# Optimization experiments

Measured on AMD Instinct MI355X. Metric: run time of the kernel, lower is better.

Reference implementation:

```python
import jax, jax.numpy as jnp
import numpy as np

N_ATOMS = 100_000
N_PAIRS = 3_200_000
N_SPECIES = 8
BOX = 5.0


def _sym(key, lo, hi):
    m = jax.random.uniform(key, (N_SPECIES, N_SPECIES), minval=lo, maxval=hi, dtype=jnp.float32)
    return 0.5 * (m + m.T)  # species matrices must be symmetric


def setup_inputs() -> dict:
    key = jax.random.key(0)
    ks = jax.random.split(key, 7)
    positions = jax.random.uniform(ks[0], (N_ATOMS, 3), dtype=jnp.float32) * BOX
    cell = BOX * jnp.eye(3, dtype=jnp.float32)
    i = jax.random.randint(ks[1], (N_PAIRS,), 0, N_ATOMS)
    off = jax.random.randint(ks[2], (N_PAIRS,), 1, N_ATOMS)  # exclude self-pairs (r=0)
    j = (i + off) % N_ATOMS
    mapping = jnp.stack([i, j]).astype(jnp.int64)
    shifts = jnp.zeros((N_PAIRS, 3), dtype=jnp.float32)
    species = jax.random.randint(ks[3], (N_ATOMS,), 0, N_SPECIES).astype(jnp.int64)
    sigma_matrix = _sym(ks[4], 1.0, 2.0)
    epsilon_matrix = _sym(ks[5], 0.5, 1.5)
    alpha_matrix = _sym(ks[6], 2.0, 3.0)
    return dict(positions=positions, cell=cell, sigma_matrix=sigma_matrix,
                epsilon_matrix=epsilon_matrix, alpha_matrix=alpha_matrix,
                shifts=shifts, mapping=mapping, species=species)


def reference(positions, cell, sigma_matrix, epsilon_matrix, alpha_matrix, shifts, mapping, species):
    n = positions.shape[0]
    i, j = mapping[0], mapping[1]
    # pair displacements with periodic shifts: dr = r_j - r_i + S @ cell
    dr = positions[j] - positions[i] + shifts @ cell              # [P,3]
    r = jnp.sqrt(jnp.sum(dr * dr, axis=-1))                       # [P]
    # species-pair parameter lookup
    si, sj = species[i], species[j]
    sigma = sigma_matrix[si, sj]
    eps = epsilon_matrix[si, sj]
    alpha = alpha_matrix[si, sj]
    # soft-sphere pair energy: eps/alpha * (1 - r/sigma)^alpha for r < sigma, else 0
    mask = r < sigma
    base = jnp.where(mask, 1.0 - r / sigma, 1.0)                  # safe base for pow/grad
    e_pair = jnp.where(mask, (eps / alpha) * base ** alpha, 0.0)
    energy = 0.5 * jnp.sum(e_pair)
    energies = (jax.ops.segment_sum(0.5 * e_pair, i, num_segments=n)
                + jax.ops.segment_sum(0.5 * e_pair, j, num_segments=n))
    # pair force magnitude: -dE/dr = eps/sigma * (1 - r/sigma)^(alpha-1)
    f_pair = jnp.where(mask, (eps / sigma) * base ** (alpha - 1.0), 0.0)
    fvec = (f_pair / r)[:, None] * dr                             # [P,3]
    forces = (jax.ops.segment_sum(fvec, i, num_segments=n)
              - jax.ops.segment_sum(fvec, j, num_segments=n))
    # virial stress
    volume = jnp.abs(jnp.linalg.det(cell))
    stress = -jnp.einsum('pi,pj->ij', dr, fvec) / volume          # [3,3]
    return energy, energies, forces, stress
```

## Files before the change

kernel.cpp:

```cpp
#include <hip/hip_runtime.h>
#include <math.h>

#define NSP 8

typedef float v4f __attribute__((ext_vector_type(4)));

#define FSCALE 1048576.0f
#define FINV   (1.0f/1048576.0f)
#define ESCALE 131072.0f
#define EINV   (1.0f/131072.0f)
#define FBIAS  2.0f

__global__ __launch_bounds__(256) void repack_kernel(
    const float* __restrict__ pos, const int* __restrict__ spec,
    v4f* __restrict__ ps, unsigned long long* __restrict__ accum, int n)
{
    int t = blockIdx.x * blockDim.x + threadIdx.x;
    if (t < n) {
        v4f v;
        v.x = pos[3 * t];
        v.y = pos[3 * t + 1];
        v.z = pos[3 * t + 2];
        v.w = __int_as_float(spec[t]);
        ps[t] = v;
        accum[2 * t]     = 0ULL;
        accum[2 * t + 1] = 0ULL;
    }
}

__global__ __launch_bounds__(256, 8) void pair_kernel(
    const v4f* __restrict__ ps,
    const float* __restrict__ cell,
    const float* __restrict__ sigma_m,
    const float* __restrict__ eps_m,
    const float* __restrict__ alpha_m,
    const float* __restrict__ shifts,
    const int* __restrict__ mapping,
    unsigned long long* __restrict__ accum,
    float* __restrict__ partials,
    int n_atoms, int n_pairs)
{
    __shared__ float s_sigma[64], s_invsig[64], s_alpha[64], s_eoa[64], s_eos[64];
    __shared__ float s_cell[9];
    const int t = threadIdx.x;
    if (t < 64) {
        float sg = sigma_m[t], ep = eps_m[t], al = alpha_m[t];
        s_sigma[t]  = sg;
        s_invsig[t] = 1.0f / sg;
        s_alpha[t]  = al;
        s_eoa[t]    = ep / al;
        s_eos[t]    = ep / sg;
    }
    if (t < 9) s_cell[t] = cell[t];
    __syncthreads();

    const int p = blockIdx.x * 256 + t;

    float le = 0.f;
    float s00 = 0.f, s01 = 0.f, s02 = 0.f, s11 = 0.f, s12 = 0.f, s22 = 0.f;

    if (p < n_pairs) {
        const int i = mapping[p];
        const int j = mapping[p + n_pairs];
        const float shx = shifts[3 * p];
        const float shy = shifts[3 * p + 1];
        const float shz = shifts[3 * p + 2];

        const v4f pi = ps[i];
        const v4f pj = ps[j];

        const float drx = pj.x - pi.x + shx * s_cell[0] + shy * s_cell[3] + shz * s_cell[6];
        const float dry = pj.y - pi.y + shx * s_cell[1] + shy * s_cell[4] + shz * s_cell[7];
        const float drz = pj.z - pi.z + shx * s_cell[2] + shy * s_cell[5] + shz * s_cell[8];
        const float r = sqrtf(drx * drx + dry * dry + drz * drz);

        const int idx = __float_as_int(pi.w) * NSP + __float_as_int(pj.w);
        const float sg = s_sigma[idx];
        if (r < sg) {
            const float base = 1.0f - r * s_invsig[idx];
            const float pb   = __powf(base, s_alpha[idx] - 1.0f);
            const float e    = s_eoa[idx] * pb * base;
            const float f    = s_eos[idx] * pb;
            const float sc   = f / r;
            const float fx = sc * drx, fy = sc * dry, fz = sc * drz;

            le  = e;
            s00 = drx * fx; s01 = drx * fy; s02 = drx * fz;
            s11 = dry * fy; s12 = dry * fz; s22 = drz * fz;

            const float he = 0.5f * e;
            const unsigned long long he_fix = (unsigned long long)__float2uint_rn(he * ESCALE);
            {
                const unsigned long long fxq = (unsigned long long)__float2uint_rn((fx + FBIAS) * FSCALE);
                const unsigned long long fyq = (unsigned long long)__float2uint_rn((fy + FBIAS) * FSCALE);
                const unsigned long long fzq = (unsigned long long)__float2uint_rn((fz + FBIAS) * FSCALE);
                atomicAdd(&accum[2 * i],     (fxq << 32) | fyq);
                atomicAdd(&accum[2 * i + 1], (1ULL << 56) | (he_fix << 32) | fzq);
            }
            {
                const unsigned long long fxq = (unsigned long long)__float2uint_rn((FBIAS - fx) * FSCALE);
                const unsigned long long fyq = (unsigned long long)__float2uint_rn((FBIAS - fy) * FSCALE);
                const unsigned long long fzq = (unsigned long long)__float2uint_rn((FBIAS - fz) * FSCALE);
                atomicAdd(&accum[2 * j],     (fxq << 32) | fyq);
                atomicAdd(&accum[2 * j + 1], (1ULL << 56) | (he_fix << 32) | fzq);
            }
        }
    }

    float vals[7] = {le, s00, s01, s02, s11, s12, s22};
    #pragma unroll
    for (int k = 0; k < 7; ++k) {
        float v = vals[k];
        #pragma unroll
        for (int off = 32; off > 0; off >>= 1)
            v += __shfl_down(v, off, 64);
        vals[k] = v;
    }
    __shared__ float s_red[4][7];
    const int wave = t >> 6, lane = t & 63;
    if (lane == 0) {
        #pragma unroll
        for (int k = 0; k < 7; ++k) s_red[wave][k] = vals[k];
    }
    __syncthreads();
    if (t == 0) {
        #pragma unroll
        for (int k = 0; k < 7; ++k) {
            partials[(size_t)blockIdx.x * 8 + k] =
                s_red[0][k] + s_red[1][k] + s_red[2][k] + s_red[3][k];
        }
        partials[(size_t)blockIdx.x * 8 + 7] = 0.f;
    }
}

__global__ __launch_bounds__(256) void reduce_tail(
    const float* __restrict__ partials, float* __restrict__ tail, int nblocks)
{
    const int t = threadIdx.x;
    float acc[7] = {0.f, 0.f, 0.f, 0.f, 0.f, 0.f, 0.f};
    for (int b = t; b < nblocks; b += 256) {
        #pragma unroll
        for (int k = 0; k < 7; ++k) acc[k] += partials[(size_t)b * 8 + k];
    }
    #pragma unroll
    for (int k = 0; k < 7; ++k) {
        float v = acc[k];
        #pragma unroll
        for (int off = 32; off > 0; off >>= 1)
            v += __shfl_down(v, off, 64);
        acc[k] = v;
    }
    __shared__ float s_red[4][7];
    const int wave = t >> 6, lane = t & 63;
    if (lane == 0) {
        #pragma unroll
        for (int k = 0; k < 7; ++k) s_red[wave][k] = acc[k];
    }
    __syncthreads();
    if (t == 0) {
        #pragma unroll
        for (int k = 0; k < 7; ++k)
            tail[k] = s_red[0][k] + s_red[1][k] + s_red[2][k] + s_red[3][k];
    }
}

__global__ __launch_bounds__(256) void finalize_kernel(
    const unsigned long long* __restrict__ accum, const float* __restrict__ tail,
    const float* __restrict__ cell, float* __restrict__ out, int n_atoms)
{
    const int t = blockIdx.x * blockDim.x + threadIdx.x;
    if (t < n_atoms) {
        const unsigned long long A = accum[2 * t];
        const unsigned long long B = accum[2 * t + 1];
        const float cntb = (float)(unsigned)(B >> 56) * FBIAS;
        const float fx = (float)(unsigned)(A >> 32)          * FINV - cntb;
        const float fy = (float)(unsigned)(A & 0xFFFFFFFFu)  * FINV - cntb;
        const float fz = (float)(unsigned)(B & 0xFFFFFFFFu)  * FINV - cntb;
        const float he = (float)(unsigned)((B >> 32) & 0xFFFFFFu) * EINV;
        out[1 + t] = he;
        float* forces = out + 1 + n_atoms;
        forces[3 * t]     = fx;
        forces[3 * t + 1] = fy;
        forces[3 * t + 2] = fz;
    }
    if (t == 0) {
        out[0] = 0.5f * tail[0];
        const float c0 = cell[0], c1 = cell[1], c2 = cell[2];
        const float c3 = cell[3], c4 = cell[4], c5 = cell[5];
        const float c6 = cell[6], c7 = cell[7], c8 = cell[8];
        const float det = c0 * (c4 * c8 - c5 * c7)
                        - c1 * (c3 * c8 - c5 * c6)
                        + c2 * (c3 * c7 - c4 * c6);
        const float nv = -1.0f / fabsf(det);
        float* st = out + 1 + 4 * n_atoms;
        st[0] = tail[1] * nv;  st[1] = tail[2] * nv;  st[2] = tail[3] * nv;
        st[3] = tail[2] * nv;  st[4] = tail[4] * nv;  st[5] = tail[5] * nv;
        st[6] = tail[3] * nv;  st[7] = tail[5] * nv;  st[8] = tail[6] * nv;
    }
}

__global__ __launch_bounds__(256) void soft_sphere_fallback(
    const float* __restrict__ positions, const float* __restrict__ cell,
    const float* __restrict__ sigma_m, const float* __restrict__ eps_m,
    const float* __restrict__ alpha_m, const float* __restrict__ shifts,
    const int* __restrict__ mapping, const int* __restrict__ species,
    float* __restrict__ out, int n_atoms, int n_pairs)
{
    __shared__ float s_sigma[64], s_invsig[64], s_alpha[64], s_eoa[64], s_eos[64];
    __shared__ float s_cell[9];
    const int t = threadIdx.x;
    if (t < 64) {
        float sg = sigma_m[t], ep = eps_m[t], al = alpha_m[t];
        s_sigma[t] = sg; s_invsig[t] = 1.0f / sg; s_alpha[t] = al;
        s_eoa[t] = ep / al; s_eos[t] = ep / sg;
    }
    if (t < 9) s_cell[t] = cell[t];
    __syncthreads();

    float* energies = out + 1;
    float* forces   = out + 1 + n_atoms;
    float* stress   = out + 1 + 4 * n_atoms;

    float le = 0.f, s00 = 0.f, s01 = 0.f, s02 = 0.f, s11 = 0.f, s12 = 0.f, s22 = 0.f;
    const int stride = blockDim.x * gridDim.x;
    for (int p = blockIdx.x * blockDim.x + t; p < n_pairs; p += stride) {
        const int i = mapping[p], j = mapping[p + n_pairs];
        const float drx = positions[3*j]   - positions[3*i]   + shifts[3*p]*s_cell[0] + shifts[3*p+1]*s_cell[3] + shifts[3*p+2]*s_cell[6];
        const float dry = positions[3*j+1] - positions[3*i+1] + shifts[3*p]*s_cell[1] + shifts[3*p+1]*s_cell[4] + shifts[3*p+2]*s_cell[7];
        const float drz = positions[3*j+2] - positions[3*i+2] + shifts[3*p]*s_cell[2] + shifts[3*p+1]*s_cell[5] + shifts[3*p+2]*s_cell[8];
        const float r = sqrtf(drx*drx + dry*dry + drz*drz);
        const int idx = species[i] * NSP + species[j];
        if (r < s_sigma[idx]) {
            const float base = 1.0f - r * s_invsig[idx];
            const float pb = __powf(base, s_alpha[idx] - 1.0f);
            const float e = s_eoa[idx] * pb * base;
            const float sc = s_eos[idx] * pb / r;
            const float fx = sc*drx, fy = sc*dry, fz = sc*drz;
            le += e;
            s00 += drx*fx; s01 += drx*fy; s02 += drx*fz;
            s11 += dry*fy; s12 += dry*fz; s22 += drz*fz;
            atomicAdd(&energies[i], 0.5f*e); atomicAdd(&energies[j], 0.5f*e);
            atomicAdd(&forces[3*i], fx); atomicAdd(&forces[3*i+1], fy); atomicAdd(&forces[3*i+2], fz);
            atomicAdd(&forces[3*j], -fx); atomicAdd(&forces[3*j+1], -fy); atomicAdd(&forces[3*j+2], -fz);
        }
    }
    float vals[7] = {le, s00, s01, s02, s11, s12, s22};
    #pragma unroll
    for (int k = 0; k < 7; ++k) {
        float v = vals[k];
        #pragma unroll
        for (int off = 32; off > 0; off >>= 1) v += __shfl_down(v, off, 64);
        vals[k] = v;
    }
    __shared__ float s_red[4][7];
    const int wave = t >> 6, lane = t & 63;
    if (lane == 0) for (int k = 0; k < 7; ++k) s_red[wave][k] = vals[k];
    __syncthreads();
    if (t == 0) {
        const int nwaves = blockDim.x >> 6;
        float tot[7];
        for (int k = 0; k < 7; ++k) {
            float v = s_red[0][k];
            for (int w = 1; w < nwaves; ++w) v += s_red[w][k];
            tot[k] = v;
        }
        atomicAdd(&out[0], 0.5f * tot[0]);
        const float det = s_cell[0]*(s_cell[4]*s_cell[8]-s_cell[5]*s_cell[7])
                        - s_cell[1]*(s_cell[3]*s_cell[8]-s_cell[5]*s_cell[6])
                        + s_cell[2]*(s_cell[3]*s_cell[7]-s_cell[4]*s_cell[6]);
        const float nv = -1.0f / fabsf(det);
        atomicAdd(&stress[0], tot[1]*nv); atomicAdd(&stress[1], tot[2]*nv); atomicAdd(&stress[2], tot[3]*nv);
        atomicAdd(&stress[3], tot[2]*nv); atomicAdd(&stress[4], tot[4]*nv); atomicAdd(&stress[5], tot[5]*nv);
        atomicAdd(&stress[6], tot[3]*nv); atomicAdd(&stress[7], tot[5]*nv); atomicAdd(&stress[8], tot[6]*nv);
    }
}

extern "C" void kernel_launch(void* const* d_in, const int* in_sizes, int n_in,
                              void* d_out, int out_size, void* d_ws, size_t ws_size,
                              hipStream_t stream) {
    const float* positions = (const float*)d_in[0];
    const float* cell      = (const float*)d_in[1];
    const float* sigma_m   = (const float*)d_in[2];
    const float* eps_m     = (const float*)d_in[3];
    const float* alpha_m   = (const float*)d_in[4];
    const float* shifts    = (const float*)d_in[5];
    const int*   mapping   = (const int*)d_in[6];
    const int*   species   = (const int*)d_in[7];
    float* out = (float*)d_out;

    const int n_atoms = in_sizes[0] / 3;
    const int n_pairs = in_sizes[6] / 2;

    const int pk_blocks = (n_pairs + 255) / 256;

    const size_t off_accum = 0;
    const size_t off_ps    = off_accum + (size_t)n_atoms * 16;
    const size_t off_part  = off_ps    + (size_t)n_atoms * 16;
    const size_t off_tail  = off_part  + (((size_t)pk_blocks * 32 + 15) & ~15ULL);
    const size_t need      = off_tail + 64;

    if (ws_size < need) {
        hipMemsetAsync(d_out, 0, (size_t)out_size * sizeof(float), stream);
        int blocks = ((n_pairs + 3) / 4 + 255) / 256;
        soft_sphere_fallback<<<blocks, 256, 0, stream>>>(
            positions, cell, sigma_m, eps_m, alpha_m, shifts, mapping, species,
            out, n_atoms, n_pairs);
        return;
    }

    char* wsb = (char*)d_ws;
    unsigned long long* accum    = (unsigned long long*)(wsb + off_accum);
    v4f*                ps       = (v4f*)(wsb + off_ps);
    float*              partials = (float*)(wsb + off_part);
    float*              tail     = (float*)(wsb + off_tail);

    const int rp_blocks = (n_atoms + 255) / 256;
    repack_kernel<<<rp_blocks, 256, 0, stream>>>(positions, species, ps, accum, n_atoms);

    pair_kernel<<<pk_blocks, 256, 0, stream>>>(
        ps, cell, sigma_m, eps_m, alpha_m, shifts, mapping,
        accum, partials, n_atoms, n_pairs);

    reduce_tail<<<1, 256, 0, stream>>>(partials, tail, pk_blocks);

    finalize_kernel<<<rp_blocks, 256, 0, stream>>>(accum, tail, cell, out, n_atoms);
}
```

Before: 172.8 us.

## Use shared-memory atomics for block reduction and fold tail reduce into finalize

```diff
diff --git a/kernel.cpp b/kernel.cpp
--- a/kernel.cpp
+++ b/kernel.cpp
@@ -13,7 +13,7 @@
 
 __global__ __launch_bounds__(256) void repack_kernel(
     const float* __restrict__ pos, const int* __restrict__ spec,
-    v4f* __restrict__ ps, unsigned long long* __restrict__ accum, int n)
+    v4f* __restrict__ ps, int n)
 {
     int t = blockIdx.x * blockDim.x + threadIdx.x;
     if (t < n) {
@@ -23,8 +23,6 @@
         v.z = pos[3 * t + 2];
         v.w = __int_as_float(spec[t]);
         ps[t] = v;
-        accum[2 * t]     = 0ULL;
-        accum[2 * t + 1] = 0ULL;
     }
 }
 
@@ -42,6 +40,7 @@
 {
     __shared__ float s_sigma[64], s_invsig[64], s_alpha[64], s_eoa[64], s_eos[64];
     __shared__ float s_cell[9];
+    __shared__ float s_acc[8];
     const int t = threadIdx.x;
     if (t < 64) {
         float sg = sigma_m[t], ep = eps_m[t], al = alpha_m[t];
@@ -52,12 +51,10 @@
         s_eos[t]    = ep / sg;
     }
     if (t < 9) s_cell[t] = cell[t];
+    if (t < 8) s_acc[t] = 0.f;
     __syncthreads();
 
     const int p = blockIdx.x * 256 + t;
-
-    float le = 0.f;
-    float s00 = 0.f, s01 = 0.f, s02 = 0.f, s11 = 0.f, s12 = 0.f, s22 = 0.f;
 
     if (p < n_pairs) {
         const int i = mapping[p];
@@ -84,9 +81,13 @@
             const float sc   = f / r;
             const float fx = sc * drx, fy = sc * dry, fz = sc * drz;
 
-            le  = e;
-            s00 = drx * fx; s01 = drx * fy; s02 = drx * fz;
-            s11 = dry * fy; s12 = dry * fz; s22 = drz * fz;
+            atomicAdd(&s_acc[0], e);
+            atomicAdd(&s_acc[1], drx * fx);
+            atomicAdd(&s_acc[2], drx * fy);
+            atomicAdd(&s_acc[3], drx * fz);
+            atomicAdd(&s_acc[4], dry * fy);
+            atomicAdd(&s_acc[5], dry * fz);
+            atomicAdd(&s_acc[6], drz * fz);
 
             const float he = 0.5f * e;
             const unsigned long long he_fix = (unsigned long long)__float2uint_rn(he * ESCALE);
@@ -107,95 +108,62 @@
         }
     }
 
-    float vals[7] = {le, s00, s01, s02, s11, s12, s22};
-    #pragma unroll
-    for (int k = 0; k < 7; ++k) {
-        float v = vals[k];
-        #pragma unroll
-        for (int off = 32; off > 0; off >>= 1)
-            v += __shfl_down(v, off, 64);
-        vals[k] = v;
-    }
-    __shared__ float s_red[4][7];
-    const int wave = t >> 6, lane = t & 63;
-    if (lane == 0) {
-        #pragma unroll
-        for (int k = 0; k < 7; ++k) s_red[wave][k] = vals[k];
-    }
-    __syncthreads();
-    if (t == 0) {
-        #pragma unroll
-        for (int k = 0; k < 7; ++k) {
-            partials[(size_t)blockIdx.x * 8 + k] =
-                s_red[0][k] + s_red[1][k] + s_red[2][k] + s_red[3][k];
-        }
-        partials[(size_t)blockIdx.x * 8 + 7] = 0.f;
-    }
-}
-
-__global__ __launch_bounds__(256) void reduce_tail(
-    const float* __restrict__ partials, float* __restrict__ tail, int nblocks)
-{
-    const int t = threadIdx.x;
-    float acc[7] = {0.f, 0.f, 0.f, 0.f, 0.f, 0.f, 0.f};
-    for (int b = t; b < nblocks; b += 256) {
-        #pragma unroll
-        for (int k = 0; k < 7; ++k) acc[k] += partials[(size_t)b * 8 + k];
-    }
-    #pragma unroll
-    for (int k = 0; k < 7; ++k) {
-        float v = acc[k];
-        #pragma unroll
-        for (int off = 32; off > 0; off >>= 1)
-            v += __shfl_down(v, off, 64);
-        acc[k] = v;
-    }
-    __shared__ float s_red[4][7];
-    const int wave = t >> 6, lane = t & 63;
-    if (lane == 0) {
-        #pragma unroll
-        for (int k = 0; k < 7; ++k) s_red[wave][k] = acc[k];
-    }
-    __syncthreads();
-    if (t == 0) {
-        #pragma unroll
-        for (int k = 0; k < 7; ++k)
-            tail[k] = s_red[0][k] + s_red[1][k] + s_red[2][k] + s_red[3][k];
-    }
+    __syncthreads();
+    if (t < 8) partials[(size_t)blockIdx.x * 8 + t] = s_acc[t];
 }
 
 __global__ __launch_bounds__(256) void finalize_kernel(
-    const unsigned long long* __restrict__ accum, const float* __restrict__ tail,
+    const unsigned long long* __restrict__ accum,
+    const float* __restrict__ partials, int nblocks,
     const float* __restrict__ cell, float* __restrict__ out, int n_atoms)
 {
-    const int t = blockIdx.x * blockDim.x + threadIdx.x;
-    if (t < n_atoms) {
-        const unsigned long long A = accum[2 * t];
-        const unsigned long long B = accum[2 * t + 1];
-        const float cntb = (float)(unsigned)(B >> 56) * FBIAS;
-        const float fx = (float)(unsigned)(A >> 32)          * FINV - cntb;
-        const float fy = (float)(unsigned)(A & 0xFFFFFFFFu)  * FINV - cntb;
-        const float fz = (float)(unsigned)(B & 0xFFFFFFFFu)  * FINV - cntb;
-        const float he = (float)(unsigned)((B >> 32) & 0xFFFFFFu) * EINV;
-        out[1 + t] = he;
-        float* forces = out + 1 + n_atoms;
-        forces[3 * t]     = fx;
-        forces[3 * t + 1] = fy;
-        forces[3 * t + 2] = fz;
-    }
-    if (t == 0) {
-        out[0] = 0.5f * tail[0];
-        const float c0 = cell[0], c1 = cell[1], c2 = cell[2];
-        const float c3 = cell[3], c4 = cell[4], c5 = cell[5];
-        const float c6 = cell[6], c7 = cell[7], c8 = cell[8];
-        const float det = c0 * (c4 * c8 - c5 * c7)
-                        - c1 * (c3 * c8 - c5 * c6)
-                        + c2 * (c3 * c7 - c4 * c6);
-        const float nv = -1.0f / fabsf(det);
-        float* st = out + 1 + 4 * n_atoms;
-        st[0] = tail[1] * nv;  st[1] = tail[2] * nv;  st[2] = tail[3] * nv;
-        st[3] = tail[2] * nv;  st[4] = tail[4] * nv;  st[5] = tail[5] * nv;
-        st[6] = tail[3] * nv;  st[7] = tail[5] * nv;  st[8] = tail[6] * nv;
+    if (blockIdx.x == 0) {
+        __shared__ float s_tail[8];
+        const int t = threadIdx.x;
+        if (t < 8) s_tail[t] = 0.f;
+        __syncthreads();
+        float a0 = 0.f, a1 = 0.f, a2 = 0.f, a3 = 0.f, a4 = 0.f, a5 = 0.f, a6 = 0.f;
+        for (int b = t; b < nblocks; b += 256) {
+            const v4f lo = *(const v4f*)(partials + (size_t)b * 8);
+            const v4f hi = *(const v4f*)(partials + (size_t)b * 8 + 4);
+            a0 += lo.x; a1 += lo.y; a2 += lo.z; a3 += lo.w;
+            a4 += hi.x; a5 += hi.y; a6 += hi.z;
+        }
+        atomicAdd(&s_tail[0], a0); atomicAdd(&s_tail[1], a1);
+        atomicAdd(&s_tail[2], a2); atomicAdd(&s_tail[3], a3);
+        atomicAdd(&s_tail[4], a4); atomicAdd(&s_tail[5], a5);
+        atomicAdd(&s_tail[6], a6);
+        __syncthreads();
+        if (t == 0) {
+            out[0] = 0.5f * s_tail[0];
+            const float c0 = cell[0], c1 = cell[1], c2 = cell[2];
+            const float c3 = cell[3], c4 = cell[4], c5 = cell[5];
+            const float c6 = cell[6], c7 = cell[7], c8 = cell[8];
+            const float det = c0 * (c4 * c8 - c5 * c7)
+                            - c1 * (c3 * c8 - c5 * c6)
+                            + c2 * (c3 * c7 - c4 * c6);
+            const float nv = -1.0f / fabsf(det);
+            float* st = out + 1 + 4 * n_atoms;
+            st[0] = s_tail[1] * nv;  st[1] = s_tail[2] * nv;  st[2] = s_tail[3] * nv;
+            st[3] = s_tail[2] * nv;  st[4] = s_tail[4] * nv;  st[5] = s_tail[5] * nv;
+            st[6] = s_tail[3] * nv;  st[7] = s_tail[5] * nv;  st[8] = s_tail[6] * nv;
+        }
+    } else {
+        const int t = (blockIdx.x - 1) * 256 + threadIdx.x;
+        if (t < n_atoms) {
+            const unsigned long long A = accum[2 * t];
+            const unsigned long long B = accum[2 * t + 1];
+            const float cntb = (float)(unsigned)(B >> 56) * FBIAS;
+            const float fx = (float)(unsigned)(A >> 32)          * FINV - cntb;
+            const float fy = (float)(unsigned)(A & 0xFFFFFFFFu)  * FINV - cntb;
+            const float fz = (float)(unsigned)(B & 0xFFFFFFFFu)  * FINV - cntb;
+            const float he = (float)(unsigned)((B >> 32) & 0xFFFFFFu) * EINV;
+            out[1 + t] = he;
+            float* forces = out + 1 + n_atoms;
+            forces[3 * t]     = fx;
+            forces[3 * t + 1] = fy;
+            forces[3 * t + 2] = fz;
+        }
     }
 }
 
@@ -292,12 +260,12 @@
     const int n_pairs = in_sizes[6] / 2;
 
     const int pk_blocks = (n_pairs + 255) / 256;
+    const int rp_blocks = (n_atoms + 255) / 256;
 
     const size_t off_accum = 0;
-    const size_t off_ps    = off_accum + (size_t)n_atoms * 16;
-    const size_t off_part  = off_ps    + (size_t)n_atoms * 16;
-    const size_t off_tail  = off_part  + (((size_t)pk_blocks * 32 + 15) & ~15ULL);
-    const size_t need      = off_tail + 64;
+    const size_t off_part  = off_accum + (size_t)n_atoms * 16;
+    const size_t off_ps    = off_part  + (((size_t)pk_blocks * 32 + 15) & ~15ULL);
+    const size_t need      = off_ps + (size_t)n_atoms * 16;
 
     if (ws_size < need) {
         hipMemsetAsync(d_out, 0, (size_t)out_size * sizeof(float), stream);
@@ -310,18 +278,17 @@
 
     char* wsb = (char*)d_ws;
     unsigned long long* accum    = (unsigned long long*)(wsb + off_accum);
+    float*              partials = (float*)(wsb + off_part);
     v4f*                ps       = (v4f*)(wsb + off_ps);
-    float*              partials = (float*)(wsb + off_part);
-    float*              tail     = (float*)(wsb + off_tail);
-
-    const int rp_blocks = (n_atoms + 255) / 256;
-    repack_kernel<<<rp_blocks, 256, 0, stream>>>(positions, species, ps, accum, n_atoms);
+
+    hipMemsetAsync(accum, 0, (size_t)n_atoms * 16, stream);
+
+    repack_kernel<<<rp_blocks, 256, 0, stream>>>(positions, species, ps, n_atoms);
 
     pair_kernel<<<pk_blocks, 256, 0, stream>>>(
         ps, cell, sigma_m, eps_m, alpha_m, shifts, mapping,
         accum, partials, n_atoms, n_pairs);
 
-    reduce_tail<<<1, 256, 0, stream>>>(partials, tail, pk_blocks);
-
-    finalize_kernel<<<rp_blocks, 256, 0, stream>>>(accum, tail, cell, out, n_atoms);
-}
+    finalize_kernel<<<1 + rp_blocks, 256, 0, stream>>>(
+        accum, partials, pk_blocks, cell, out, n_atoms);
+}
```

Result: slower. 191.2 us (+10.6%).

## Fuse repack, pair, and finalize stages into one cooperative persistent kernel

Applied to the files above, without the earlier changes.

```diff
diff --git a/kernel.cpp b/kernel.cpp
--- a/kernel.cpp
+++ b/kernel.cpp
@@ -1,5 +1,8 @@
 #include <hip/hip_runtime.h>
+#include <hip/hip_cooperative_groups.h>
 #include <math.h>
+
+namespace cg = cooperative_groups;
 
 #define NSP 8
 
@@ -10,6 +13,183 @@
 #define ESCALE 131072.0f
 #define EINV   (1.0f/131072.0f)
 #define FBIAS  2.0f
+
+__global__ __launch_bounds__(256, 8) void fused_kernel(
+    const float* __restrict__ pos, const int* __restrict__ spec,
+    const float* __restrict__ cell,
+    const float* __restrict__ sigma_m, const float* __restrict__ eps_m,
+    const float* __restrict__ alpha_m,
+    const float* __restrict__ shifts, const int* __restrict__ mapping,
+    v4f* __restrict__ ps, unsigned long long* __restrict__ accum,
+    float* __restrict__ partials, float* __restrict__ out,
+    int n_atoms, int n_pairs)
+{
+    cg::grid_group grid = cg::this_grid();
+
+    __shared__ float s_sigma[64], s_invsig[64], s_alpha[64], s_eoa[64], s_eos[64];
+    __shared__ float s_cell[9];
+    const int t = threadIdx.x;
+    if (t < 64) {
+        float sg = sigma_m[t], ep = eps_m[t], al = alpha_m[t];
+        s_sigma[t]  = sg;
+        s_invsig[t] = 1.0f / sg;
+        s_alpha[t]  = al;
+        s_eoa[t]    = ep / al;
+        s_eos[t]    = ep / sg;
+    }
+    if (t < 9) s_cell[t] = cell[t];
+    __syncthreads();
+
+    const int gsize = gridDim.x * 256;
+    const int gtid  = blockIdx.x * 256 + t;
+
+    for (int a = gtid; a < n_atoms; a += gsize) {
+        v4f v;
+        v.x = pos[3 * a];
+        v.y = pos[3 * a + 1];
+        v.z = pos[3 * a + 2];
+        v.w = __int_as_float(spec[a]);
+        ps[a] = v;
+        accum[2 * a]     = 0ULL;
+        accum[2 * a + 1] = 0ULL;
+    }
+    grid.sync();
+
+    float le = 0.f;
+    float s00 = 0.f, s01 = 0.f, s02 = 0.f, s11 = 0.f, s12 = 0.f, s22 = 0.f;
+
+    for (int p = gtid; p < n_pairs; p += gsize) {
+        const int i = mapping[p];
+        const int j = mapping[p + n_pairs];
+        const float shx = shifts[3 * p];
+        const float shy = shifts[3 * p + 1];
+        const float shz = shifts[3 * p + 2];
+
+        const v4f pi = ps[i];
+        const v4f pj = ps[j];
+
+        const float drx = pj.x - pi.x + shx * s_cell[0] + shy * s_cell[3] + shz * s_cell[6];
+        const float dry = pj.y - pi.y + shx * s_cell[1] + shy * s_cell[4] + shz * s_cell[7];
+        const float drz = pj.z - pi.z + shx * s_cell[2] + shy * s_cell[5] + shz * s_cell[8];
+        const float r = sqrtf(drx * drx + dry * dry + drz * drz);
+
+        const int idx = __float_as_int(pi.w) * NSP + __float_as_int(pj.w);
+        const float sg = s_sigma[idx];
+        if (r < sg) {
+            const float base = 1.0f - r * s_invsig[idx];
+            const float pb   = __powf(base, s_alpha[idx] - 1.0f);
+            const float e    = s_eoa[idx] * pb * base;
+            const float f    = s_eos[idx] * pb;
+            const float sc   = f / r;
+            const float fx = sc * drx, fy = sc * dry, fz = sc * drz;
+
+            le  += e;
+            s00 += drx * fx; s01 += drx * fy; s02 += drx * fz;
+            s11 += dry * fy; s12 += dry * fz; s22 += drz * fz;
+
+            const float he = 0.5f * e;
+            const unsigned long long he_fix = (unsigned long long)__float2uint_rn(he * ESCALE);
+            {
+                const unsigned long long fxq = (unsigned long long)__float2uint_rn((fx + FBIAS) * FSCALE);
+                const unsigned long long fyq = (unsigned long long)__float2uint_rn((fy + FBIAS) * FSCALE);
+                const unsigned long long fzq = (unsigned long long)__float2uint_rn((fz + FBIAS) * FSCALE);
+                atomicAdd(&accum[2 * i],     (fxq << 32) | fyq);
+                atomicAdd(&accum[2 * i + 1], (1ULL << 56) | (he_fix << 32) | fzq);
+            }
+            {
+                const unsigned long long fxq = (unsigned long long)__float2uint_rn((FBIAS - fx) * FSCALE);
+                const unsigned long long fyq = (unsigned long long)__float2uint_rn((FBIAS - fy) * FSCALE);
+                const unsigned long long fzq = (unsigned long long)__float2uint_rn((FBIAS - fz) * FSCALE);
+                atomicAdd(&accum[2 * j],     (fxq << 32) | fyq);
+                atomicAdd(&accum[2 * j + 1], (1ULL << 56) | (he_fix << 32) | fzq);
+            }
+        }
+    }
+
+    {
+        float vals[7] = {le, s00, s01, s02, s11, s12, s22};
+        #pragma unroll
+        for (int k = 0; k < 7; ++k) {
+            float v = vals[k];
+            #pragma unroll
+            for (int off = 32; off > 0; off >>= 1)
+                v += __shfl_down(v, off, 64);
+            vals[k] = v;
+        }
+        __shared__ float s_red[4][7];
+        const int wave = t >> 6, lane = t & 63;
+        if (lane == 0) {
+            #pragma unroll
+            for (int k = 0; k < 7; ++k) s_red[wave][k] = vals[k];
+        }
+        __syncthreads();
+        if (t < 8) {
+            float v = 0.f;
+            if (t < 7) v = s_red[0][t] + s_red[1][t] + s_red[2][t] + s_red[3][t];
+            partials[(size_t)blockIdx.x * 8 + t] = v;
+        }
+    }
+    grid.sync();
+
+    for (int a = gtid; a < n_atoms; a += gsize) {
+        const unsigned long long A = accum[2 * a];
+        const unsigned long long B = accum[2 * a + 1];
+        const float cntb = (float)(unsigned)(B >> 56) * FBIAS;
+        const float fx = (float)(unsigned)(A >> 32)          * FINV - cntb;
+        const float fy = (float)(unsigned)(A & 0xFFFFFFFFu)  * FINV - cntb;
+        const float fz = (float)(unsigned)(B & 0xFFFFFFFFu)  * FINV - cntb;
+        const float he = (float)(unsigned)((B >> 32) & 0xFFFFFFu) * EINV;
+        out[1 + a] = he;
+        float* forces = out + 1 + n_atoms;
+        forces[3 * a]     = fx;
+        forces[3 * a + 1] = fy;
+        forces[3 * a + 2] = fz;
+    }
+
+    if (blockIdx.x == 0) {
+        float a0 = 0.f, a1 = 0.f, a2 = 0.f, a3 = 0.f, a4 = 0.f, a5 = 0.f, a6 = 0.f;
+        for (int b = t; b < (int)gridDim.x; b += 256) {
+            const v4f lo = *(const v4f*)(partials + (size_t)b * 8);
+            const v4f hi = *(const v4f*)(partials + (size_t)b * 8 + 4);
+            a0 += lo.x; a1 += lo.y; a2 += lo.z; a3 += lo.w;
+            a4 += hi.x; a5 += hi.y; a6 += hi.z;
+        }
+        float vals[7] = {a0, a1, a2, a3, a4, a5, a6};
+        #pragma unroll
+        for (int k = 0; k < 7; ++k) {
+            float v = vals[k];
+            #pragma unroll
+            for (int off = 32; off > 0; off >>= 1)
+                v += __shfl_down(v, off, 64);
+            vals[k] = v;
+        }
+        __shared__ float s_red2[4][7];
+        const int wave = t >> 6, lane = t & 63;
+        if (lane == 0) {
+            #pragma unroll
+            for (int k = 0; k < 7; ++k) s_red2[wave][k] = vals[k];
+        }
+        __syncthreads();
+        if (t == 0) {
+            float tot[7];
+            #pragma unroll
+            for (int k = 0; k < 7; ++k)
+                tot[k] = s_red2[0][k] + s_red2[1][k] + s_red2[2][k] + s_red2[3][k];
+            out[0] = 0.5f * tot[0];
+            const float c0 = s_cell[0], c1 = s_cell[1], c2 = s_cell[2];
+            const float c3 = s_cell[3], c4 = s_cell[4], c5 = s_cell[5];
+            const float c6 = s_cell[6], c7 = s_cell[7], c8 = s_cell[8];
+            const float det = c0 * (c4 * c8 - c5 * c7)
+                            - c1 * (c3 * c8 - c5 * c6)
+                            + c2 * (c3 * c7 - c4 * c6);
+            const float nv = -1.0f / fabsf(det);
+            float* st = out + 1 + 4 * n_atoms;
+            st[0] = tot[1] * nv;  st[1] = tot[2] * nv;  st[2] = tot[3] * nv;
+            st[3] = tot[2] * nv;  st[4] = tot[4] * nv;  st[5] = tot[5] * nv;
+            st[6] = tot[3] * nv;  st[7] = tot[5] * nv;  st[8] = tot[6] * nv;
+        }
+    }
+}
 
 __global__ __launch_bounds__(256) void repack_kernel(
     const float* __restrict__ pos, const int* __restrict__ spec,
@@ -55,9 +235,7 @@
     __syncthreads();
 
     const int p = blockIdx.x * 256 + t;
-
-    float le = 0.f;
-    float s00 = 0.f, s01 = 0.f, s02 = 0.f, s11 = 0.f, s12 = 0.f, s22 = 0.f;
+    float le = 0.f, s00 = 0.f, s01 = 0.f, s02 = 0.f, s11 = 0.f, s12 = 0.f, s22 = 0.f;
 
     if (p < n_pairs) {
         const int i = mapping[p];
@@ -65,29 +243,22 @@
         const float shx = shifts[3 * p];
         const float shy = shifts[3 * p + 1];
         const float shz = shifts[3 * p + 2];
-
         const v4f pi = ps[i];
         const v4f pj = ps[j];
-
         const float drx = pj.x - pi.x + shx * s_cell[0] + shy * s_cell[3] + shz * s_cell[6];
         const float dry = pj.y - pi.y + shx * s_cell[1] + shy * s_cell[4] + shz * s_cell[7];
         const float drz = pj.z - pi.z + shx * s_cell[2] + shy * s_cell[5] + shz * s_cell[8];
         const float r = sqrtf(drx * drx + dry * dry + drz * drz);
-
         const int idx = __float_as_int(pi.w) * NSP + __float_as_int(pj.w);
-        const float sg = s_sigma[idx];
-        if (r < sg) {
+        if (r < s_sigma[idx]) {
             const float base = 1.0f - r * s_invsig[idx];
             const float pb   = __powf(base, s_alpha[idx] - 1.0f);
             const float e    = s_eoa[idx] * pb * base;
-            const float f    = s_eos[idx] * pb;
-            const float sc   = f / r;
+            const float sc   = s_eos[idx] * pb / r;
             const float fx = sc * drx, fy = sc * dry, fz = sc * drz;
-
             le  = e;
             s00 = drx * fx; s01 = drx * fy; s02 = drx * fz;
             s11 = dry * fy; s12 = dry * fz; s22 = drz * fz;
-
             const float he = 0.5f * e;
             const unsigned long long he_fix = (unsigned long long)__float2uint_rn(he * ESCALE);
             {
@@ -123,79 +294,65 @@
         for (int k = 0; k < 7; ++k) s_red[wave][k] = vals[k];
     }
     __syncthreads();
-    if (t == 0) {
-        #pragma unroll
-        for (int k = 0; k < 7; ++k) {
-            partials[(size_t)blockIdx.x * 8 + k] =
-                s_red[0][k] + s_red[1][k] + s_red[2][k] + s_red[3][k];
-        }
-        partials[(size_t)blockIdx.x * 8 + 7] = 0.f;
+    if (t < 8) {
+        float v = 0.f;
+        if (t < 7) v = s_red[0][t] + s_red[1][t] + s_red[2][t] + s_red[3][t];
+        partials[(size_t)blockIdx.x * 8 + t] = v;
     }
 }
 
-__global__ __launch_bounds__(256) void reduce_tail(
-    const float* __restrict__ partials, float* __restrict__ tail, int nblocks)
-{
-    const int t = threadIdx.x;
-    float acc[7] = {0.f, 0.f, 0.f, 0.f, 0.f, 0.f, 0.f};
-    for (int b = t; b < nblocks; b += 256) {
-        #pragma unroll
-        for (int k = 0; k < 7; ++k) acc[k] += partials[(size_t)b * 8 + k];
-    }
-    #pragma unroll
-    for (int k = 0; k < 7; ++k) {
-        float v = acc[k];
-        #pragma unroll
-        for (int off = 32; off > 0; off >>= 1)
-            v += __shfl_down(v, off, 64);
-        acc[k] = v;
-    }
-    __shared__ float s_red[4][7];
-    const int wave = t >> 6, lane = t & 63;
-    if (lane == 0) {
-        #pragma unroll
-        for (int k = 0; k < 7; ++k) s_red[wave][k] = acc[k];
-    }
-    __syncthreads();
-    if (t == 0) {
-        #pragma unroll
-        for (int k = 0; k < 7; ++k)
-            tail[k] = s_red[0][k] + s_red[1][k] + s_red[2][k] + s_red[3][k];
-    }
-}
-
 __global__ __launch_bounds__(256) void finalize_kernel(
-    const unsigned long long* __restrict__ accum, const float* __restrict__ tail,
+    const unsigned long long* __restrict__ accum,
+    const float* __restrict__ partials, int nblocks,
     const float* __restrict__ cell, float* __restrict__ out, int n_atoms)
 {
-    const int t = blockIdx.x * blockDim.x + threadIdx.x;
-    if (t < n_atoms) {
-        const unsigned long long A = accum[2 * t];
-        const unsigned long long B = accum[2 * t + 1];
-        const float cntb = (float)(unsigned)(B >> 56) * FBIAS;
-        const float fx = (float)(unsigned)(A >> 32)          * FINV - cntb;
-        const float fy = (float)(unsigned)(A & 0xFFFFFFFFu)  * FINV - cntb;
-        const float fz = (float)(unsigned)(B & 0xFFFFFFFFu)  * FINV - cntb;
-        const float he = (float)(unsigned)((B >> 32) & 0xFFFFFFu) * EINV;
-        out[1 + t] = he;
-        float* forces = out + 1 + n_atoms;
-        forces[3 * t]     = fx;
-        forces[3 * t + 1] = fy;
-        forces[3 * t + 2] = fz;
-    }
-    if (t == 0) {
-        out[0] = 0.5f * tail[0];
-        const float c0 = cell[0], c1 = cell[1], c2 = cell[2];
-        const float c3 = cell[3], c4 = cell[4], c5 = cell[5];
-        const float c6 = cell[6], c7 = cell[7], c8 = cell[8];
-        const float det = c0 * (c4 * c8 - c5 * c7)
-                        - c1 * (c3 * c8 - c5 * c6)
-                        + c2 * (c3 * c7 - c4 * c6);
-        const float nv = -1.0f / fabsf(det);
-        float* st = out + 1 + 4 * n_atoms;
-        st[0] = tail[1] * nv;  st[1] = tail[2] * nv;  st[2] = tail[3] * nv;
-        st[3] = tail[2] * nv;  st[4] = tail[4] * nv;  st[5] = tail[5] * nv;
-        st[6] = tail[3] * nv;  st[7] = tail[5] * nv;  st[8] = tail[6] * nv;
+    if (blockIdx.x == 0) {
+        __shared__ float s_tail[8];
+        const int t = threadIdx.x;
+        if (t < 8) s_tail[t] = 0.f;
+        __syncthreads();
+        float a0 = 0.f, a1 = 0.f, a2 = 0.f, a3 = 0.f, a4 = 0.f, a5 = 0.f, a6 = 0.f;
+        for (int b = t; b < nblocks; b += 256) {
+            const v4f lo = *(const v4f*)(partials + (size_t)b * 8);
+            const v4f hi = *(const v4f*)(partials + (size_t)b * 8 + 4);
+            a0 += lo.x; a1 += lo.y; a2 += lo.z; a3 += lo.w;
+            a4 += hi.x; a5 += hi.y; a6 += hi.z;
+        }
+        atomicAdd(&s_tail[0], a0); atomicAdd(&s_tail[1], a1);
+        atomicAdd(&s_tail[2], a2); atomicAdd(&s_tail[3], a3);
+        atomicAdd(&s_tail[4], a4); atomicAdd(&s_tail[5], a5);
+        atomicAdd(&s_tail[6], a6);
+        __syncthreads();
+        if (t == 0) {
+            out[0] = 0.5f * s_tail[0];
+            const float c0 = cell[0], c1 = cell[1], c2 = cell[2];
+            const float c3 = cell[3], c4 = cell[4], c5 = cell[5];
+            const float c6 = cell[6], c7 = cell[7], c8 = cell[8];
+            const float det = c0 * (c4 * c8 - c5 * c7)
+                            - c1 * (c3 * c8 - c5 * c6)
+                            + c2 * (c3 * c7 - c4 * c6);
+            const float nv = -1.0f / fabsf(det);
+            float* st = out + 1 + 4 * n_atoms;
+            st[0] = s_tail[1] * nv;  st[1] = s_tail[2] * nv;  st[2] = s_tail[3] * nv;
+            st[3] = s_tail[2] * nv;  st[4] = s_tail[4] * nv;  st[5] = s_tail[5] * nv;
+            st[6] = s_tail[3] * nv;  st[7] = s_tail[5] * nv;  st[8] = s_tail[6] * nv;
+        }
+    } else {
+        const int t = (blockIdx.x - 1) * 256 + threadIdx.x;
+        if (t < n_atoms) {
+            const unsigned long long A = accum[2 * t];
+            const unsigned long long B = accum[2 * t + 1];
+            const float cntb = (float)(unsigned)(B >> 56) * FBIAS;
+            const float fx = (float)(unsigned)(A >> 32)          * FINV - cntb;
+            const float fy = (float)(unsigned)(A & 0xFFFFFFFFu)  * FINV - cntb;
+            const float fz = (float)(unsigned)(B & 0xFFFFFFFFu)  * FINV - cntb;
+            const float he = (float)(unsigned)((B >> 32) & 0xFFFFFFu) * EINV;
+            out[1 + t] = he;
+            float* forces = out + 1 + n_atoms;
+            forces[3 * t]     = fx;
+            forces[3 * t + 1] = fy;
+            forces[3 * t + 2] = fz;
+        }
     }
 }
 
@@ -292,12 +449,13 @@
     const int n_pairs = in_sizes[6] / 2;
 
     const int pk_blocks = (n_pairs + 255) / 256;
-
+    const int rp_blocks = (n_atoms + 255) / 256;
+
+    const size_t part_cap  = ((size_t)(pk_blocks > 4096 ? pk_blocks : 4096)) * 32;
     const size_t off_accum = 0;
     const size_t off_ps    = off_accum + (size_t)n_atoms * 16;
     const size_t off_part  = off_ps    + (size_t)n_atoms * 16;
-    const size_t off_tail  = off_part  + (((size_t)pk_blocks * 32 + 15) & ~15ULL);
-    const size_t need      = off_tail + 64;
+    const size_t need      = off_part + part_cap;
 
     if (ws_size < need) {
         hipMemsetAsync(d_out, 0, (size_t)out_size * sizeof(float), stream);
@@ -312,16 +470,42 @@
     unsigned long long* accum    = (unsigned long long*)(wsb + off_accum);
     v4f*                ps       = (v4f*)(wsb + off_ps);
     float*              partials = (float*)(wsb + off_part);
-    float*              tail     = (float*)(wsb + off_tail);
-
-    const int rp_blocks = (n_atoms + 255) / 256;
-    repack_kernel<<<rp_blocks, 256, 0, stream>>>(positions, species, ps, accum, n_atoms);
-
-    pair_kernel<<<pk_blocks, 256, 0, stream>>>(
-        ps, cell, sigma_m, eps_m, alpha_m, shifts, mapping,
-        accum, partials, n_atoms, n_pairs);
-
-    reduce_tail<<<1, 256, 0, stream>>>(partials, tail, pk_blocks);
-
-    finalize_kernel<<<rp_blocks, 256, 0, stream>>>(accum, tail, cell, out, n_atoms);
+
+    int coop = 0, numCU = 0, dev = 0;
+    (void)hipGetDevice(&dev);
+    (void)hipDeviceGetAttribute(&coop, hipDeviceAttributeCooperativeLaunch, dev);
+    (void)hipDeviceGetAttribute(&numCU, hipDeviceAttributeMultiprocessorCount, dev);
+
+    bool launched = false;
+    if (coop && numCU > 0) {
+        int blocksPerCU = 0;
+        if (hipOccupancyMaxActiveBlocksPerMultiprocessor(
+                &blocksPerCU, (const void*)fused_kernel, 256, 0) == hipSuccess
+            && blocksPerCU > 0) {
+            int nblocks = blocksPerCU * numCU;
+            if (nblocks > pk_blocks) nblocks = pk_blocks;
+            if (nblocks > 0) {
+                void* args[] = {
+                    (void*)&positions, (void*)&species, (void*)&cell,
+                    (void*)&sigma_m, (void*)&eps_m, (void*)&alpha_m,
+                    (void*)&shifts, (void*)&mapping,
+                    (void*)&ps, (void*)&accum, (void*)&partials, (void*)&out,
+                    (void*)&n_atoms, (void*)&n_pairs
+                };
+                hipError_t err = hipLaunchCooperativeKernel(
+                    (const void*)fused_kernel, dim3(nblocks), dim3(256),
+                    args, 0, stream);
+                launched = (err == hipSuccess);
+            }
+        }
+    }
+
+    if (!launched) {
+        repack_kernel<<<rp_blocks, 256, 0, stream>>>(positions, species, ps, accum, n_atoms);
+        pair_kernel<<<pk_blocks, 256, 0, stream>>>(
+            ps, cell, sigma_m, eps_m, alpha_m, shifts, mapping,
+            accum, partials, n_atoms, n_pairs);
+        finalize_kernel<<<1 + rp_blocks, 256, 0, stream>>>(
+            accum, partials, pk_blocks, cell, out, n_atoms);
+    }
 }
```

Result: slower. 393.8 us (+127.8%).

## Replace packed fixed-point atomics with direct float atomics and last-block reduction

Applied to the files above, without the earlier changes.

```diff
diff --git a/kernel.cpp b/kernel.cpp
--- a/kernel.cpp
+++ b/kernel.cpp
@@ -2,30 +2,27 @@
 #include <math.h>
 
 #define NSP 8
+#define NSLOT 256
 
 typedef float v4f __attribute__((ext_vector_type(4)));
 
-#define FSCALE 1048576.0f
-#define FINV   (1.0f/1048576.0f)
-#define ESCALE 131072.0f
-#define EINV   (1.0f/131072.0f)
-#define FBIAS  2.0f
-
-__global__ __launch_bounds__(256) void repack_kernel(
+__global__ __launch_bounds__(256) void init_kernel(
     const float* __restrict__ pos, const int* __restrict__ spec,
-    v4f* __restrict__ ps, unsigned long long* __restrict__ accum, int n)
+    v4f* __restrict__ ps, float* __restrict__ slots ,
+    float* __restrict__ out, int n_atoms, int out_sz)
 {
-    int t = blockIdx.x * blockDim.x + threadIdx.x;
-    if (t < n) {
+    const int t  = blockIdx.x * 256 + threadIdx.x;
+    const int gs = gridDim.x * 256;
+    for (int a = t; a < n_atoms; a += gs) {
         v4f v;
-        v.x = pos[3 * t];
-        v.y = pos[3 * t + 1];
-        v.z = pos[3 * t + 2];
-        v.w = __int_as_float(spec[t]);
-        ps[t] = v;
-        accum[2 * t]     = 0ULL;
-        accum[2 * t + 1] = 0ULL;
-    }
+        v.x = pos[3 * a];
+        v.y = pos[3 * a + 1];
+        v.z = pos[3 * a + 2];
+        v.w = __int_as_float(spec[a]);
+        ps[a] = v;
+    }
+    for (int k = t; k < out_sz; k += gs) out[k] = 0.f;
+    for (int k = t; k < NSLOT * 32 + 32; k += gs) slots[k] = 0.f;
 }
 
 __global__ __launch_bounds__(256, 8) void pair_kernel(
@@ -36,8 +33,8 @@
     const float* __restrict__ alpha_m,
     const float* __restrict__ shifts,
     const int* __restrict__ mapping,
-    unsigned long long* __restrict__ accum,
-    float* __restrict__ partials,
+    float* __restrict__ slots,
+    float* __restrict__ out,
     int n_atoms, int n_pairs)
 {
     __shared__ float s_sigma[64], s_invsig[64], s_alpha[64], s_eoa[64], s_eos[64];
@@ -55,9 +52,10 @@
     __syncthreads();
 
     const int p = blockIdx.x * 256 + t;
-
-    float le = 0.f;
-    float s00 = 0.f, s01 = 0.f, s02 = 0.f, s11 = 0.f, s12 = 0.f, s22 = 0.f;
+    float le = 0.f, s00 = 0.f, s01 = 0.f, s02 = 0.f, s11 = 0.f, s12 = 0.f, s22 = 0.f;
+
+    float* __restrict__ energies = out + 1;
+    float* __restrict__ forces   = out + 1 + n_atoms;
 
     if (p < n_pairs) {
         const int i = mapping[p];
@@ -75,13 +73,11 @@
         const float r = sqrtf(drx * drx + dry * dry + drz * drz);
 
         const int idx = __float_as_int(pi.w) * NSP + __float_as_int(pj.w);
-        const float sg = s_sigma[idx];
-        if (r < sg) {
+        if (r < s_sigma[idx]) {
             const float base = 1.0f - r * s_invsig[idx];
             const float pb   = __powf(base, s_alpha[idx] - 1.0f);
             const float e    = s_eoa[idx] * pb * base;
-            const float f    = s_eos[idx] * pb;
-            const float sc   = f / r;
+            const float sc   = s_eos[idx] * pb / r;
             const float fx = sc * drx, fy = sc * dry, fz = sc * drz;
 
             le  = e;
@@ -89,113 +85,89 @@
             s11 = dry * fy; s12 = dry * fz; s22 = drz * fz;
 
             const float he = 0.5f * e;
-            const unsigned long long he_fix = (unsigned long long)__float2uint_rn(he * ESCALE);
-            {
-                const unsigned long long fxq = (unsigned long long)__float2uint_rn((fx + FBIAS) * FSCALE);
-                const unsigned long long fyq = (unsigned long long)__float2uint_rn((fy + FBIAS) * FSCALE);
-                const unsigned long long fzq = (unsigned long long)__float2uint_rn((fz + FBIAS) * FSCALE);
-                atomicAdd(&accum[2 * i],     (fxq << 32) | fyq);
-                atomicAdd(&accum[2 * i + 1], (1ULL << 56) | (he_fix << 32) | fzq);
-            }
-            {
-                const unsigned long long fxq = (unsigned long long)__float2uint_rn((FBIAS - fx) * FSCALE);
-                const unsigned long long fyq = (unsigned long long)__float2uint_rn((FBIAS - fy) * FSCALE);
-                const unsigned long long fzq = (unsigned long long)__float2uint_rn((FBIAS - fz) * FSCALE);
-                atomicAdd(&accum[2 * j],     (fxq << 32) | fyq);
-                atomicAdd(&accum[2 * j + 1], (1ULL << 56) | (he_fix << 32) | fzq);
-            }
-        }
-    }
-
-    float vals[7] = {le, s00, s01, s02, s11, s12, s22};
-    #pragma unroll
-    for (int k = 0; k < 7; ++k) {
-        float v = vals[k];
-        #pragma unroll
-        for (int off = 32; off > 0; off >>= 1)
-            v += __shfl_down(v, off, 64);
-        vals[k] = v;
-    }
-    __shared__ float s_red[4][7];
-    const int wave = t >> 6, lane = t & 63;
-    if (lane == 0) {
-        #pragma unroll
-        for (int k = 0; k < 7; ++k) s_red[wave][k] = vals[k];
-    }
+            atomicAdd(&energies[i], he);
+            atomicAdd(&energies[j], he);
+            atomicAdd(&forces[3 * i],     fx);
+            atomicAdd(&forces[3 * i + 1], fy);
+            atomicAdd(&forces[3 * i + 2], fz);
+            atomicAdd(&forces[3 * j],     -fx);
+            atomicAdd(&forces[3 * j + 1], -fy);
+            atomicAdd(&forces[3 * j + 2], -fz);
+        }
+    }
+
+    {
+        float vals[7] = {le, s00, s01, s02, s11, s12, s22};
+        #pragma unroll
+        for (int k = 0; k < 7; ++k) {
+            float v = vals[k];
+            #pragma unroll
+            for (int off = 32; off > 0; off >>= 1)
+                v += __shfl_down(v, off, 64);
+            vals[k] = v;
+        }
+        __shared__ float s_red[4][7];
+        const int wave = t >> 6, lane = t & 63;
+        if (lane == 0) {
+            #pragma unroll
+            for (int k = 0; k < 7; ++k) s_red[wave][k] = vals[k];
+        }
+        __syncthreads();
+        if (t < 7) {
+            const float v = s_red[0][t] + s_red[1][t] + s_red[2][t] + s_red[3][t];
+            atomicAdd(&slots[(size_t)(blockIdx.x & (NSLOT - 1)) * 32 + t], v);
+        }
+    }
+
+    __shared__ unsigned s_last;
     __syncthreads();
     if (t == 0) {
+        __threadfence();
+        unsigned* ticket = (unsigned*)(slots + (size_t)NSLOT * 32);
+        const unsigned old = atomicAdd(ticket, 1u);
+        s_last = (old == gridDim.x - 1) ? 1u : 0u;
+    }
+    __syncthreads();
+
+    if (s_last) {
+        __threadfence();
+        float vals[7];
+        #pragma unroll
+        for (int k = 0; k < 7; ++k)
+            vals[k] = atomicAdd(&slots[(size_t)t * 32 + k], 0.0f);
         #pragma unroll
         for (int k = 0; k < 7; ++k) {
-            partials[(size_t)blockIdx.x * 8 + k] =
-                s_red[0][k] + s_red[1][k] + s_red[2][k] + s_red[3][k];
-        }
-        partials[(size_t)blockIdx.x * 8 + 7] = 0.f;
-    }
-}
-
-__global__ __launch_bounds__(256) void reduce_tail(
-    const float* __restrict__ partials, float* __restrict__ tail, int nblocks)
-{
-    const int t = threadIdx.x;
-    float acc[7] = {0.f, 0.f, 0.f, 0.f, 0.f, 0.f, 0.f};
-    for (int b = t; b < nblocks; b += 256) {
-        #pragma unroll
-        for (int k = 0; k < 7; ++k) acc[k] += partials[(size_t)b * 8 + k];
-    }
-    #pragma unroll
-    for (int k = 0; k < 7; ++k) {
-        float v = acc[k];
-        #pragma unroll
-        for (int off = 32; off > 0; off >>= 1)
-            v += __shfl_down(v, off, 64);
-        acc[k] = v;
-    }
-    __shared__ float s_red[4][7];
-    const int wave = t >> 6, lane = t & 63;
-    if (lane == 0) {
-        #pragma unroll
-        for (int k = 0; k < 7; ++k) s_red[wave][k] = acc[k];
-    }
-    __syncthreads();
-    if (t == 0) {
-        #pragma unroll
-        for (int k = 0; k < 7; ++k)
-            tail[k] = s_red[0][k] + s_red[1][k] + s_red[2][k] + s_red[3][k];
-    }
-}
-
-__global__ __launch_bounds__(256) void finalize_kernel(
-    const unsigned long long* __restrict__ accum, const float* __restrict__ tail,
-    const float* __restrict__ cell, float* __restrict__ out, int n_atoms)
-{
-    const int t = blockIdx.x * blockDim.x + threadIdx.x;
-    if (t < n_atoms) {
-        const unsigned long long A = accum[2 * t];
-        const unsigned long long B = accum[2 * t + 1];
-        const float cntb = (float)(unsigned)(B >> 56) * FBIAS;
-        const float fx = (float)(unsigned)(A >> 32)          * FINV - cntb;
-        const float fy = (float)(unsigned)(A & 0xFFFFFFFFu)  * FINV - cntb;
-        const float fz = (float)(unsigned)(B & 0xFFFFFFFFu)  * FINV - cntb;
-        const float he = (float)(unsigned)((B >> 32) & 0xFFFFFFu) * EINV;
-        out[1 + t] = he;
-        float* forces = out + 1 + n_atoms;
-        forces[3 * t]     = fx;
-        forces[3 * t + 1] = fy;
-        forces[3 * t + 2] = fz;
-    }
-    if (t == 0) {
-        out[0] = 0.5f * tail[0];
-        const float c0 = cell[0], c1 = cell[1], c2 = cell[2];
-        const float c3 = cell[3], c4 = cell[4], c5 = cell[5];
-        const float c6 = cell[6], c7 = cell[7], c8 = cell[8];
-        const float det = c0 * (c4 * c8 - c5 * c7)
-                        - c1 * (c3 * c8 - c5 * c6)
-                        + c2 * (c3 * c7 - c4 * c6);
-        const float nv = -1.0f / fabsf(det);
-        float* st = out + 1 + 4 * n_atoms;
-        st[0] = tail[1] * nv;  st[1] = tail[2] * nv;  st[2] = tail[3] * nv;
-        st[3] = tail[2] * nv;  st[4] = tail[4] * nv;  st[5] = tail[5] * nv;
-        st[6] = tail[3] * nv;  st[7] = tail[5] * nv;  st[8] = tail[6] * nv;
+            float v = vals[k];
+            #pragma unroll
+            for (int off = 32; off > 0; off >>= 1)
+                v += __shfl_down(v, off, 64);
+            vals[k] = v;
+        }
+        __shared__ float s_red2[4][7];
+        const int wave = t >> 6, lane = t & 63;
+        if (lane == 0) {
+            #pragma unroll
+            for (int k = 0; k < 7; ++k) s_red2[wave][k] = vals[k];
+        }
+        __syncthreads();
+        if (t == 0) {
+            float tot[7];
+            #pragma unroll
+            for (int k = 0; k < 7; ++k)
+                tot[k] = s_red2[0][k] + s_red2[1][k] + s_red2[2][k] + s_red2[3][k];
+            out[0] = 0.5f * tot[0];
+            const float c0 = s_cell[0], c1 = s_cell[1], c2 = s_cell[2];
+            const float c3 = s_cell[3], c4 = s_cell[4], c5 = s_cell[5];
+            const float c6 = s_cell[6], c7 = s_cell[7], c8 = s_cell[8];
+            const float det = c0 * (c4 * c8 - c5 * c7)
+                            - c1 * (c3 * c8 - c5 * c6)
+                            + c2 * (c3 * c7 - c4 * c6);
+            const float nv = -1.0f / fabsf(det);
+            float* st = out + 1 + 4 * n_atoms;
+            st[0] = tot[1] * nv;  st[1] = tot[2] * nv;  st[2] = tot[3] * nv;
+            st[3] = tot[2] * nv;  st[4] = tot[4] * nv;  st[5] = tot[5] * nv;
+            st[6] = tot[3] * nv;  st[7] = tot[5] * nv;  st[8] = tot[6] * nv;
+        }
     }
 }
 
@@ -291,13 +263,9 @@
     const int n_atoms = in_sizes[0] / 3;
     const int n_pairs = in_sizes[6] / 2;
 
-    const int pk_blocks = (n_pairs + 255) / 256;
-
-    const size_t off_accum = 0;
-    const size_t off_ps    = off_accum + (size_t)n_atoms * 16;
-    const size_t off_part  = off_ps    + (size_t)n_atoms * 16;
-    const size_t off_tail  = off_part  + (((size_t)pk_blocks * 32 + 15) & ~15ULL);
-    const size_t need      = off_tail + 64;
+    const size_t off_ps    = 0;
+    const size_t off_slots = off_ps + (size_t)n_atoms * 16;
+    const size_t need      = off_slots + (size_t)NSLOT * 32 * 4 + 128;
 
     if (ws_size < need) {
         hipMemsetAsync(d_out, 0, (size_t)out_size * sizeof(float), stream);
@@ -309,19 +277,15 @@
     }
 
     char* wsb = (char*)d_ws;
-    unsigned long long* accum    = (unsigned long long*)(wsb + off_accum);
-    v4f*                ps       = (v4f*)(wsb + off_ps);
-    float*              partials = (float*)(wsb + off_part);
-    float*              tail     = (float*)(wsb + off_tail);
-
-    const int rp_blocks = (n_atoms + 255) / 256;
-    repack_kernel<<<rp_blocks, 256, 0, stream>>>(positions, species, ps, accum, n_atoms);
-
+    v4f*   ps    = (v4f*)(wsb + off_ps);
+    float* slots = (float*)(wsb + off_slots);
+
+    const int init_blocks = (out_size + 255) / 256;
+    init_kernel<<<init_blocks, 256, 0, stream>>>(
+        positions, species, ps, slots, out, n_atoms, out_size);
+
+    const int pk_blocks = (n_pairs + 255) / 256;
     pair_kernel<<<pk_blocks, 256, 0, stream>>>(
         ps, cell, sigma_m, eps_m, alpha_m, shifts, mapping,
-        accum, partials, n_atoms, n_pairs);
-
-    reduce_tail<<<1, 256, 0, stream>>>(partials, tail, pk_blocks);
-
-    finalize_kernel<<<rp_blocks, 256, 0, stream>>>(accum, tail, cell, out, n_atoms);
-}
+        slots, out, n_atoms, n_pairs);
+}
```

Measured after the change: 493.2 us. +185.4%, slower.
